# Performance work log

Hardware: AMD Instinct MI355X
Metric: run time of the kernel (lower is better)

The kernel has to match this reference:

```python
import jax, jax.numpy as jnp
import numpy as np

FEATURE_SIZE = 1_000_000
EMBED_DIM = 64
BATCH = 16384
FIELDS = 50


def setup_inputs() -> dict:
    key = jax.random.key(0)
    k1, k2, k3 = jax.random.split(key, 3)
    feature_values = jax.random.uniform(k1, (BATCH, FIELDS), dtype=jnp.float32)
    feature_idx = jax.random.randint(k2, (BATCH, FIELDS), 0, FEATURE_SIZE, dtype=jnp.int64)
    feature_embeddings = jax.random.normal(k3, (FEATURE_SIZE, EMBED_DIM), dtype=jnp.float32)
    return {
        "feature_values": feature_values,
        "feature_idx": feature_idx,
        "feature_embeddings": feature_embeddings,
    }


def reference(feature_values, feature_idx, feature_embeddings):
    # Gather: [B, F, K]
    embeddings = feature_embeddings[feature_idx]
    # FM second-order: (sum of weighted embeddings)^2 - sum of (weighted embeddings)^2
    temp1 = jnp.square(jnp.einsum('bf,bfk->bk', feature_values, embeddings))
    temp2 = jnp.einsum('bf,bfk->bk', jnp.square(feature_values), jnp.square(embeddings))
    second_order = temp1 - temp2  # [B, K]
    return second_order
```

## Files before the change

kernel.cpp:

```cpp
#include <hip/hip_runtime.h>


constexpr int BATCH  = 16384;
constexpr int FIELDS = 50;
constexpr int EMBED  = 64;
constexpr int WAVES_PER_BLOCK = 4;

__global__ __launch_bounds__(256)
void fm_second_order_kernel(const float* __restrict__ vals,
                            const int*   __restrict__ idx,
                            const float* __restrict__ emb,
                            float* __restrict__ out)
{
    const int wave = threadIdx.x >> 6;
    const int lane = threadIdx.x & 63;
    const int b    = blockIdx.x * WAVES_PER_BLOCK + wave;
    if (b >= BATCH) return;

    const float* vrow = vals + (size_t)b * FIELDS;
    const int*   irow = idx  + (size_t)b * FIELDS;

    float acc1 = 0.0f;
    float acc2 = 0.0f;

#pragma unroll
    for (int f = 0; f < FIELDS; ++f) {
        const float v  = vrow[f];
        const int   id = irow[f];
        const float e  = emb[(size_t)id * EMBED + lane];
        const float ve = v * e;
        acc1 += ve;
        acc2 = fmaf(ve, ve, acc2);
    }

    out[(size_t)b * EMBED + lane] = fmaf(acc1, acc1, -acc2);
}

extern "C" void kernel_launch(void* const* d_in, const int* in_sizes, int n_in,
                              void* d_out, int out_size, void* d_ws, size_t ws_size,
                              hipStream_t stream) {
    const float* vals = (const float*)d_in[0];
    const int*   idx  = (const int*)d_in[1];
    const float* emb  = (const float*)d_in[2];
    float*       out  = (float*)d_out;

    const int blocks = BATCH / WAVES_PER_BLOCK;
    fm_second_order_kernel<<<blocks, WAVES_PER_BLOCK * 64, 0, stream>>>(vals, idx, emb, out);
}
```

Before: 328.3 us.

## Split wave into four field groups with float4 embedding loads and shuffle reduce

Each wave is split into four 16-lane groups. Each group handles a different field per iteration and loads a full 256-byte embedding row as float4 per lane. This cuts the serial loop from 50 gathers to 13 and issues wider vector loads. Partial sums are combined across groups with xor shuffles, and one group writes the result as float4. The cost is extra shuffle work, a padded last iteration with dummy loads from row 0, and removal of the bounds check on batch.

```diff
diff --git a/kernel.cpp b/kernel.cpp
--- a/kernel.cpp
+++ b/kernel.cpp
@@ -5,35 +5,61 @@
 constexpr int FIELDS = 50;
 constexpr int EMBED  = 64;
 constexpr int WAVES_PER_BLOCK = 4;
+constexpr int FITER  = 13;
 
 __global__ __launch_bounds__(256)
-void fm_second_order_kernel(const float* __restrict__ vals,
-                            const int*   __restrict__ idx,
-                            const float* __restrict__ emb,
-                            float* __restrict__ out)
+void fm_second_order_v2(const float* __restrict__ vals,
+                        const int*   __restrict__ idx,
+                        const float* __restrict__ emb,
+                        float* __restrict__ out)
 {
     const int wave = threadIdx.x >> 6;
     const int lane = threadIdx.x & 63;
+    const int g    = lane >> 4;
+    const int j    = lane & 15;
     const int b    = blockIdx.x * WAVES_PER_BLOCK + wave;
-    if (b >= BATCH) return;
 
     const float* vrow = vals + (size_t)b * FIELDS;
     const int*   irow = idx  + (size_t)b * FIELDS;
 
-    float acc1 = 0.0f;
-    float acc2 = 0.0f;
+    float4 s1 = make_float4(0.f, 0.f, 0.f, 0.f);
+    float4 s2 = make_float4(0.f, 0.f, 0.f, 0.f);
 
 #pragma unroll
-    for (int f = 0; f < FIELDS; ++f) {
-        const float v  = vrow[f];
-        const int   id = irow[f];
-        const float e  = emb[(size_t)id * EMBED + lane];
-        const float ve = v * e;
-        acc1 += ve;
-        acc2 = fmaf(ve, ve, acc2);
+    for (int it = 0; it < FITER; ++it) {
+        const int  f  = it * 4 + g;
+        const bool ok = (f < FIELDS);
+        const float v  = ok ? vrow[f] : 0.0f;
+        const int   id = ok ? irow[f] : 0;
+        const float4 e = *(const float4*)(emb + (size_t)id * EMBED + j * 4);
+        const float vx = v * e.x, vy = v * e.y, vz = v * e.z, vw = v * e.w;
+        s1.x += vx; s1.y += vy; s1.z += vz; s1.w += vw;
+        s2.x = fmaf(vx, vx, s2.x);
+        s2.y = fmaf(vy, vy, s2.y);
+        s2.z = fmaf(vz, vz, s2.z);
+        s2.w = fmaf(vw, vw, s2.w);
     }
 
-    out[(size_t)b * EMBED + lane] = fmaf(acc1, acc1, -acc2);
+#pragma unroll
+    for (int mask = 16; mask <= 32; mask <<= 1) {
+        s1.x += __shfl_xor(s1.x, mask, 64);
+        s1.y += __shfl_xor(s1.y, mask, 64);
+        s1.z += __shfl_xor(s1.z, mask, 64);
+        s1.w += __shfl_xor(s1.w, mask, 64);
+        s2.x += __shfl_xor(s2.x, mask, 64);
+        s2.y += __shfl_xor(s2.y, mask, 64);
+        s2.z += __shfl_xor(s2.z, mask, 64);
+        s2.w += __shfl_xor(s2.w, mask, 64);
+    }
+
+    if (g == 0) {
+        float4 r;
+        r.x = fmaf(s1.x, s1.x, -s2.x);
+        r.y = fmaf(s1.y, s1.y, -s2.y);
+        r.z = fmaf(s1.z, s1.z, -s2.z);
+        r.w = fmaf(s1.w, s1.w, -s2.w);
+        *(float4*)(out + (size_t)b * EMBED + j * 4) = r;
+    }
 }
 
 extern "C" void kernel_launch(void* const* d_in, const int* in_sizes, int n_in,
@@ -45,5 +71,5 @@
     float*       out  = (float*)d_out;
 
     const int blocks = BATCH / WAVES_PER_BLOCK;
-    fm_second_order_kernel<<<blocks, WAVES_PER_BLOCK * 64, 0, stream>>>(vals, idx, emb, out);
+    fm_second_order_v2<<<blocks, WAVES_PER_BLOCK * 64, 0, stream>>>(vals, idx, emb, out);
 }
```

Result: no change. 326.7 us (-0.5%).
